# Performance work log

Measured on AMD Instinct MI355X. Metric: run time of the kernel, lower is better.

Reference implementation:

```python
import jax, jax.numpy as jnp
import numpy as np

N_NODES = 100000
N_USERS = 60000
N_MOVIES = 40000
N_EDGES = 1200000
D_IN = 64
D_EMB = 64


def setup_inputs() -> dict:
    key = jax.random.key(0)
    ks = jax.random.split(key, 6)
    x = jax.random.normal(ks[0], (N_NODES, D_IN), dtype=jnp.float32)
    edge_index = jax.random.randint(ks[1], (2, N_EDGES), 0, N_NODES, dtype=jnp.int64)
    # Glorot-ish init for the two GCNConv linear weights
    W1 = jax.random.normal(ks[2], (D_IN, D_EMB), dtype=jnp.float32) * (1.0 / np.sqrt(D_IN))
    b1 = jnp.zeros((D_EMB,), dtype=jnp.float32)
    W2 = jax.random.normal(ks[3], (D_EMB, D_EMB), dtype=jnp.float32) * (1.0 / np.sqrt(D_EMB))
    b2 = jnp.zeros((D_EMB,), dtype=jnp.float32)
    return {"x": x, "edge_index": edge_index, "W1": W1, "b1": b1, "W2": W2, "b2": b2}


def gcn_conv(x, W, b, src, dst):
    """PyG GCNConv: D^{-1/2}(A+I)D^{-1/2} X W + b with symmetric norm and self-loops."""
    h = x @ W  # [N, D_out]
    ones = jnp.ones(src.shape[0], dtype=h.dtype)
    # degree includes self-loop (+1)
    deg = jax.ops.segment_sum(ones, dst, num_segments=N_NODES) + 1.0
    dinv = jax.lax.rsqrt(deg)  # [N]
    coef = dinv[src] * dinv[dst]  # [E]
    agg = jax.ops.segment_sum(h[src] * coef[:, None], dst, num_segments=N_NODES)
    # self-loop contribution: norm = dinv[i]^2
    return agg + h * (dinv * dinv)[:, None] + b


def reference(x, edge_index, W1, b1, W2, b2):
    src, dst = edge_index[0], edge_index[1]
    h = gcn_conv(x, W1, b1, src, dst)
    h = jax.nn.relu(h)  # dropout is identity in eval mode
    h = gcn_conv(h, W2, b2, src, dst)
    user = h[:N_USERS]
    movie = h[N_USERS:N_USERS + N_MOVIES]
    return user, movie, h
```

## Files before the change

### kernel.cpp

```cpp
#include <hip/hip_runtime.h>

#define NN 100000
#define NE 1200000
#define DD 64
#define NPART 8
#define PSZ (NN / NPART)
#define EPB 4096
#define NCHUNK ((NE + EPB - 1) / EPB)
#define SCH 1024
#define SNB ((NN + SCH - 1) / SCH)

#define KCH3 96
#define CEH3 (NE / KCH3)
#define P3 4
#define BINS3 (NN / P3)
#define BINW3 (BINS3 / 4)
#define KSEG 4
#define KPS (KCH3 / KSEG)
#define NW4 (NN / 4)
#define HISTB (KCH3 * P3)
#define GEMMB ((NN + 255) / 256)

static __device__ __forceinline__ unsigned short f2bf(float f) {
    unsigned int u = __float_as_uint(f);
    u += 0x7fffu + ((u >> 16) & 1u);
    return (unsigned short)(u >> 16);
}
static __device__ __forceinline__ float bf_lo(unsigned int u) { return __uint_as_float(u << 16); }
static __device__ __forceinline__ float bf_hi(unsigned int u) { return __uint_as_float(u & 0xffff0000u); }

__global__ __launch_bounds__(1024) void k_histgemm(const int* __restrict__ dst,
                                                   unsigned char* __restrict__ H,
                                                   unsigned char* __restrict__ rank8,
                                                   const float* __restrict__ X,
                                                   const float* __restrict__ W,
                                                   unsigned short* __restrict__ Hb) {
    __shared__ union SM {
        unsigned int bins[BINW3];
        struct { float4 Ws4[64][16]; float Xs[64][68]; } g;
    } sm;
    int t = threadIdx.x;
    if (blockIdx.x < HISTB) {
        int k = blockIdx.x >> 2;
        int p = blockIdx.x & 3;
        for (int i = t; i < BINW3; i += 1024) sm.bins[i] = 0u;
        __syncthreads();
        int lo = p * BINS3;
        int beg = k * CEH3;
        for (int e4 = beg + t * 4; e4 < beg + CEH3; e4 += 4096) {
            int4 d4 = *(const int4*)&dst[e4];
            int dd[4] = {d4.x, d4.y, d4.z, d4.w};
#pragma unroll
            for (int j = 0; j < 4; ++j) {
                unsigned int r = (unsigned int)(dd[j] - lo);
                if (r < (unsigned int)BINS3) {
                    unsigned int sh = (r & 3u) << 3;
                    unsigned int old = atomicAdd(&sm.bins[r >> 2], 1u << sh);
                    rank8[e4 + j] = (unsigned char)((old >> sh) & 0xffu);
                }
            }
        }
        __syncthreads();
        unsigned int* Hw = (unsigned int*)(H + (size_t)k * NN + lo);
        for (int i = t; i < BINW3; i += 1024) Hw[i] = sm.bins[i];
    } else {
        const float4* W4 = (const float4*)W;
        sm.g.Ws4[t >> 4][t & 15] = W4[t];
        int row0 = (int)(blockIdx.x - HISTB) * 256;
        const float4* X4 = (const float4*)X;
        int r = t >> 4, q = t & 15;
#pragma unroll
        for (int s = 0; s < 4; ++s) {
            int row = row0 + s * 64 + r;
            float4 v = make_float4(0.f, 0.f, 0.f, 0.f);
            if (row < NN) v = X4[row * 16 + q];
            __syncthreads();
            *((float4*)&sm.g.Xs[r][q * 4]) = v;
            __syncthreads();
            float4 acc = make_float4(0.f, 0.f, 0.f, 0.f);
#pragma unroll 4
            for (int k = 0; k < 64; ++k) {
                float4 w = sm.g.Ws4[k][q];
                float x = sm.g.Xs[r][k];
                acc.x += x * w.x; acc.y += x * w.y; acc.z += x * w.z; acc.w += x * w.w;
            }
            if (row < NN) {
                ushort4 o;
                o.x = f2bf(acc.x); o.y = f2bf(acc.y); o.z = f2bf(acc.z); o.w = f2bf(acc.w);
                *((ushort4*)&Hb[(size_t)row * 64 + q * 4]) = o;
            }
        }
    }
}

__global__ __launch_bounds__(256) void k_cseg_sum(const unsigned int* __restrict__ H32,
                                                  unsigned int* __restrict__ aux) {
    int wd = blockIdx.x * 256 + threadIdx.x;
    int seg = blockIdx.y;
    if (wd >= NW4) return;
    unsigned int s = 0;
#pragma unroll
    for (int k = 0; k < KPS; ++k)
        s += H32[(size_t)(seg * KPS + k) * NW4 + wd];
    aux[seg * NW4 + wd] = s;
}

__global__ __launch_bounds__(256) void k_cseg_scan2(unsigned int* __restrict__ H32,
                                                    const unsigned int* __restrict__ aux,
                                                    int* __restrict__ rowptr,
                                                    int* __restrict__ part,
                                                    float* __restrict__ dinv) {
    __shared__ int wsum[4];
    int t = threadIdx.x;
    int wd = blockIdx.x * 256 + t;
    int seg = blockIdx.y;
    bool valid = wd < NW4;
    unsigned int s = 0;
    if (valid) {
        unsigned int base = 0;
        for (int i = 0; i < seg; ++i) base += aux[i * NW4 + wd];
        s = base;
#pragma unroll
        for (int k = 0; k < KPS; ++k) {
            size_t idx = (size_t)(seg * KPS + k) * NW4 + wd;
            unsigned int v = H32[idx];
            H32[idx] = s;
            s += v;
        }
    }
    if (seg != KSEG - 1) return;
    int d0 = valid ? (int)(s & 0xffu) : 0;
    int d1 = valid ? (int)((s >> 8) & 0xffu) : 0;
    int d2 = valid ? (int)((s >> 16) & 0xffu) : 0;
    int d3 = valid ? (int)(s >> 24) : 0;
    int idx = blockIdx.x * SCH + t * 4;
    if (valid) {
        float4 dv;
        dv.x = rsqrtf((float)d0 + 1.0f);
        dv.y = rsqrtf((float)d1 + 1.0f);
        dv.z = rsqrtf((float)d2 + 1.0f);
        dv.w = rsqrtf((float)d3 + 1.0f);
        *(float4*)&dinv[idx] = dv;
    }
    int ssum = d0 + d1 + d2 + d3;
    int lane = t & 63;
    int incl = ssum;
#pragma unroll
    for (int off = 1; off < 64; off <<= 1) {
        int v = __shfl_up(incl, off);
        if (lane >= off) incl += v;
    }
    int wv = t >> 6;
    if (lane == 63) wsum[wv] = incl;
    __syncthreads();
    int woff = 0;
#pragma unroll
    for (int i = 0; i < 4; ++i) if (i < wv) woff += wsum[i];
    int excl = woff + incl - ssum;
    if (valid) {
        int4 rp = make_int4(excl, excl + d0, excl + d0 + d1, excl + d0 + d1 + d2);
        *(int4*)&rowptr[idx] = rp;
    }
    if (t == 255) part[blockIdx.x] = woff + incl;
}

__global__ __launch_bounds__(128) void k_scan_part(int* __restrict__ part, int* __restrict__ rowptr) {
    __shared__ int sm[128];
    int t = threadIdx.x;
    int v = (t < SNB) ? part[t] : 0;
    sm[t] = v;
    __syncthreads();
    for (int off = 1; off < 128; off <<= 1) {
        int add = (t >= off) ? sm[t - off] : 0;
        __syncthreads();
        sm[t] += add;
        __syncthreads();
    }
    if (t == SNB - 1) rowptr[NN] = v;
    if (t < SNB) part[t] = sm[t] - v;
}

__global__ __launch_bounds__(256) void k_fill4(const int* __restrict__ src,
                                               const int* __restrict__ dst,
                                               const unsigned char* __restrict__ rank8,
                                               const unsigned char* __restrict__ H,
                                               const int* __restrict__ rowptr,
                                               const int* __restrict__ part,
                                               const float* __restrict__ dinv,
                                               int2* __restrict__ cc) {
    int e4 = (blockIdx.x * 256 + threadIdx.x) * 4;
    if (e4 >= NE) return;
    int4 d4 = *(const int4*)&dst[e4];
    int4 s4 = *(const int4*)&src[e4];
    unsigned int r4 = *(const unsigned int*)&rank8[e4];
    int dd[4] = {d4.x, d4.y, d4.z, d4.w};
    int ss[4] = {s4.x, s4.y, s4.z, s4.w};
    int k = e4 / CEH3;
#pragma unroll
    for (int j = 0; j < 4; ++j) {
        int d = dd[j], s = ss[j];
        int base = rowptr[d] + part[d >> 10] + (int)H[(size_t)k * NN + d];
        int pos = base + (int)((r4 >> (8 * j)) & 0xffu);
        cc[pos] = make_int2(s, __float_as_int(dinv[s] * dinv[d]));
    }
}

__global__ void k_hist_rank(const int* __restrict__ dst, int* __restrict__ degi,
                            int* __restrict__ rank, int ne) {
    int i = blockIdx.x * blockDim.x + threadIdx.x;
    if (i < ne) rank[i] = atomicAdd(&degi[dst[i]], 1);
}

__global__ __launch_bounds__(256) void k_scan_local(const int* __restrict__ degi,
                                                    int* __restrict__ rowptr,
                                                    int* __restrict__ part,
                                                    float* __restrict__ dinv) {
    __shared__ int wsum[4];
    int t = threadIdx.x;
    int idx = blockIdx.x * SCH + t * 4;
    int d0 = 0, d1 = 0, d2 = 0, d3 = 0;
    if (idx + 3 < NN) {
        int4 v = *(const int4*)&degi[idx];
        d0 = v.x; d1 = v.y; d2 = v.z; d3 = v.w;
        float4 dv;
        dv.x = rsqrtf((float)d0 + 1.0f);
        dv.y = rsqrtf((float)d1 + 1.0f);
        dv.z = rsqrtf((float)d2 + 1.0f);
        dv.w = rsqrtf((float)d3 + 1.0f);
        *(float4*)&dinv[idx] = dv;
    } else {
        if (idx     < NN) { d0 = degi[idx];     dinv[idx]     = rsqrtf((float)d0 + 1.0f); }
        if (idx + 1 < NN) { d1 = degi[idx + 1]; dinv[idx + 1] = rsqrtf((float)d1 + 1.0f); }
        if (idx + 2 < NN) { d2 = degi[idx + 2]; dinv[idx + 2] = rsqrtf((float)d2 + 1.0f); }
        if (idx + 3 < NN) { d3 = degi[idx + 3]; dinv[idx + 3] = rsqrtf((float)d3 + 1.0f); }
    }
    int s = d0 + d1 + d2 + d3;
    int lane = t & 63;
    int incl = s;
#pragma unroll
    for (int off = 1; off < 64; off <<= 1) {
        int v = __shfl_up(incl, off);
        if (lane >= off) incl += v;
    }
    int wv = t >> 6;
    if (lane == 63) wsum[wv] = incl;
    __syncthreads();
    int woff = 0;
#pragma unroll
    for (int i = 0; i < 4; ++i) if (i < wv) woff += wsum[i];
    int excl = woff + incl - s;
    if (idx     < NN) rowptr[idx]     = excl;
    if (idx + 1 < NN) rowptr[idx + 1] = excl + d0;
    if (idx + 2 < NN) rowptr[idx + 2] = excl + d0 + d1;
    if (idx + 3 < NN) rowptr[idx + 3] = excl + d0 + d1 + d2;
    if (t == 255) part[blockIdx.x] = woff + incl;
}

__global__ void k_scan_add(int* __restrict__ rowptr, const int* __restrict__ part) {
    int i = blockIdx.x * blockDim.x + threadIdx.x;
    if (i < NN) rowptr[i] += part[i >> 10];
    if (i == 0) rowptr[NN] = NE;
}

__global__ void k_fill_rank(const int* __restrict__ src, const int* __restrict__ dst,
                            const int* __restrict__ rank, const int* __restrict__ rowptr,
                            int* __restrict__ csr_src, int ne) {
    int e = blockIdx.x * blockDim.x + threadIdx.x;
    if (e < ne) csr_src[rowptr[dst[e]] + rank[e]] = src[e];
}

__global__ __launch_bounds__(256) void k_pack(const int* __restrict__ rowptr,
                                              const int* __restrict__ csr,
                                              const float* __restrict__ dinv,
                                              int2* __restrict__ cc) {
    int n = blockIdx.x * 256 + threadIdx.x;
    if (n >= NN) return;
    float dn = dinv[n];
    for (int e = rowptr[n]; e < rowptr[n + 1]; ++e) {
        int s = csr[e];
        cc[e] = make_int2(s, __float_as_int(dinv[s] * dn));
    }
}

__global__ __launch_bounds__(256) void k_gemm_bf(const float* __restrict__ X,
                                                 const float* __restrict__ W,
                                                 unsigned short* __restrict__ Hb,
                                                 int nrows) {
    __shared__ float4 Ws4[64][16];
    __shared__ float  Xs[64][68];
    int tid = threadIdx.x;
    const float4* W4 = (const float4*)W;
    for (int i = tid; i < 64 * 16; i += 256) Ws4[i >> 4][i & 15] = W4[i];
    int row0 = blockIdx.x * 64;
    const float4* X4 = (const float4*)X;
    for (int i = tid; i < 64 * 16; i += 256) {
        int r = i >> 4, q = i & 15;
        int row = row0 + r;
        float4 v = make_float4(0.f, 0.f, 0.f, 0.f);
        if (row < nrows) v = X4[row * 16 + q];
        *((float4*)&Xs[r][q * 4]) = v;
    }
    __syncthreads();
    int c4 = tid & 15;
    int rg = tid >> 4;
    float4 acc0 = make_float4(0.f, 0.f, 0.f, 0.f);
    float4 acc1 = acc0, acc2 = acc0, acc3 = acc0;
#pragma unroll 4
    for (int k = 0; k < 64; ++k) {
        float4 w = Ws4[k][c4];
        float x0 = Xs[rg * 4 + 0][k];
        float x1 = Xs[rg * 4 + 1][k];
        float x2 = Xs[rg * 4 + 2][k];
        float x3 = Xs[rg * 4 + 3][k];
        acc0.x += x0 * w.x; acc0.y += x0 * w.y; acc0.z += x0 * w.z; acc0.w += x0 * w.w;
        acc1.x += x1 * w.x; acc1.y += x1 * w.y; acc1.z += x1 * w.z; acc1.w += x1 * w.w;
        acc2.x += x2 * w.x; acc2.y += x2 * w.y; acc2.z += x2 * w.z; acc2.w += x2 * w.w;
        acc3.x += x3 * w.x; acc3.y += x3 * w.y; acc3.z += x3 * w.z; acc3.w += x3 * w.w;
    }
    float4 accs[4] = {acc0, acc1, acc2, acc3};
#pragma unroll
    for (int i = 0; i < 4; ++i) {
        int row = row0 + rg * 4 + i;
        if (row < nrows) {
            ushort4 o;
            o.x = f2bf(accs[i].x); o.y = f2bf(accs[i].y);
            o.z = f2bf(accs[i].z); o.w = f2bf(accs[i].w);
            *((ushort4*)&Hb[row * 64 + c4 * 4]) = o;
        }
    }
}

static __device__ __forceinline__ void gather8(const unsigned short* __restrict__ Hb,
                                               const int2* __restrict__ cc,
                                               int e0, int deg, int dmax, int cg,
                                               float acc[8]) {
#define LDE(T, S, C) { bool _v = (T) < deg; int2 _w = _v ? cc[e0 + (T)] : make_int2(0, 0); \
                       S = _w.x; C = __int_as_float(_w.y); }
#define GAT(U, S) U = *(const uint4*)(Hb + (size_t)(S) * 64 + cg * 8);
#define CONS(U, C) { acc[0] += bf_lo(U.x) * (C);  acc[1] += bf_hi(U.x) * (C); \
                     acc[2] += bf_lo(U.y) * (C);  acc[3] += bf_hi(U.y) * (C); \
                     acc[4] += bf_lo(U.z) * (C);  acc[5] += bf_hi(U.z) * (C); \
                     acc[6] += bf_lo(U.w) * (C);  acc[7] += bf_hi(U.w) * (C); }
    int s0, s1, s2, s3; float c0, c1, c2, c3;
    LDE(0, s0, c0); LDE(1, s1, c1); LDE(2, s2, c2); LDE(3, s3, c3);
    uint4 u0, u1, u2, u3;
    GAT(u0, s0); GAT(u1, s1); GAT(u2, s2); GAT(u3, s3);
    for (int t = 0; t < dmax; t += 4) {
        int sn0, sn1, sn2, sn3; float cn0, cn1, cn2, cn3;
        LDE(t + 4, sn0, cn0); LDE(t + 5, sn1, cn1);
        LDE(t + 6, sn2, cn2); LDE(t + 7, sn3, cn3);
        CONS(u0, c0); GAT(u0, sn0); c0 = cn0;
        CONS(u1, c1); GAT(u1, sn1); c1 = cn1;
        CONS(u2, c2); GAT(u2, sn2); c2 = cn2;
        CONS(u3, c3); GAT(u3, sn3); c3 = cn3;
    }
#undef LDE
#undef GAT
#undef CONS
}

__global__ __launch_bounds__(256) void k_reduce_g2(const unsigned short* __restrict__ Hb,
                                                   const int* __restrict__ rowptr,
                                                   const int* __restrict__ part,
                                                   const int2* __restrict__ cc,
                                                   const float* __restrict__ dinv,
                                                   const float* __restrict__ bias,
                                                   const float* __restrict__ W2,
                                                   unsigned short* __restrict__ Hb2) {
    __shared__ float4 Ws4[64][16];
    __shared__ float rows[32][68];
    int t = threadIdx.x;
    const float4* W4 = (const float4*)W2;
    for (int i = t; i < 1024; i += 256) Ws4[i >> 4][i & 15] = W4[i];

    int n = blockIdx.x * 32 + (t >> 3);
    int cg = t & 7;
    bool nv = n < NN;
    float din = nv ? dinv[n] : 0.f;
    uint4 us = make_uint4(0u, 0u, 0u, 0u);
    int e0 = 0, deg = 0;
    if (nv) {
        us = *(const uint4*)(Hb + (size_t)n * 64 + cg * 8);
        int rp0 = rowptr[n] + part[n >> 10];
        int rp1 = rowptr[n + 1] + part[(n + 1) >> 10];
        e0 = rp0; deg = rp1 - rp0;
    }
    int dmax = deg;
    dmax = max(dmax, __shfl_xor(dmax, 8));
    dmax = max(dmax, __shfl_xor(dmax, 16));
    dmax = max(dmax, __shfl_xor(dmax, 32));

    float acc[8];
#pragma unroll
    for (int j = 0; j < 8; ++j) acc[j] = 0.f;
    gather8(Hb, cc, e0, deg, dmax, cg, acc);

    float ddn = din * din;
    float4 b0 = *(const float4*)(bias + cg * 8);
    float4 b1 = *(const float4*)(bias + cg * 8 + 4);
    float4 o0, o1;
    o0.x = fmaxf(acc[0] + bf_lo(us.x) * ddn + b0.x, 0.f);
    o0.y = fmaxf(acc[1] + bf_hi(us.x) * ddn + b0.y, 0.f);
    o0.z = fmaxf(acc[2] + bf_lo(us.y) * ddn + b0.z, 0.f);
    o0.w = fmaxf(acc[3] + bf_hi(us.y) * ddn + b0.w, 0.f);
    o1.x = fmaxf(acc[4] + bf_lo(us.z) * ddn + b1.x, 0.f);
    o1.y = fmaxf(acc[5] + bf_hi(us.z) * ddn + b1.y, 0.f);
    o1.z = fmaxf(acc[6] + bf_lo(us.w) * ddn + b1.z, 0.f);
    o1.w = fmaxf(acc[7] + bf_hi(us.w) * ddn + b1.w, 0.f);
    int node = t >> 3;
    *(float4*)&rows[node][cg * 8]     = o0;
    *(float4*)&rows[node][cg * 8 + 4] = o1;
    __syncthreads();

    int c2 = t & 7;
    float a0 = 0.f, a1 = 0.f, a2 = 0.f, a3 = 0.f, a4 = 0.f, a5 = 0.f, a6 = 0.f, a7 = 0.f;
#pragma unroll 4
    for (int k = 0; k < 64; ++k) {
        float r = rows[node][k];
        float4 w0 = Ws4[k][c2 * 2];
        float4 w1 = Ws4[k][c2 * 2 + 1];
        a0 += r * w0.x; a1 += r * w0.y; a2 += r * w0.z; a3 += r * w0.w;
        a4 += r * w1.x; a5 += r * w1.y; a6 += r * w1.z; a7 += r * w1.w;
    }
    if (nv) {
        uint4 pk;
        pk.x = (unsigned int)f2bf(a0) | ((unsigned int)f2bf(a1) << 16);
        pk.y = (unsigned int)f2bf(a2) | ((unsigned int)f2bf(a3) << 16);
        pk.z = (unsigned int)f2bf(a4) | ((unsigned int)f2bf(a5) << 16);
        pk.w = (unsigned int)f2bf(a6) | ((unsigned int)f2bf(a7) << 16);
        *(uint4*)&Hb2[(size_t)n * 64 + c2 * 8] = pk;
    }
}

__global__ __launch_bounds__(256) void k_reduce2(const unsigned short* __restrict__ Hb,
                                                 const int* __restrict__ rowptr,
                                                 const int* __restrict__ part,
                                                 const int2* __restrict__ cc,
                                                 const float* __restrict__ dinv,
                                                 const float* __restrict__ bias,
                                                 float* __restrict__ out0,
                                                 float* __restrict__ out1) {
    int n = blockIdx.x * 32 + (threadIdx.x >> 3);
    if (n >= NN) return;
    int cg = threadIdx.x & 7;
    float din = dinv[n];
    uint4 us = *(const uint4*)(Hb + (size_t)n * 64 + cg * 8);
    int rp0 = rowptr[n] + part[n >> 10];
    int rp1 = rowptr[n + 1] + part[(n + 1) >> 10];
    int e0 = rp0, deg = rp1 - rp0;
    int dmax = deg;
    dmax = max(dmax, __shfl_xor(dmax, 8));
    dmax = max(dmax, __shfl_xor(dmax, 16));
    dmax = max(dmax, __shfl_xor(dmax, 32));

    float acc[8];
#pragma unroll
    for (int j = 0; j < 8; ++j) acc[j] = 0.f;
    gather8(Hb, cc, e0, deg, dmax, cg, acc);

    float ddn = din * din;
    float4 b0 = *(const float4*)(bias + cg * 8);
    float4 b1 = *(const float4*)(bias + cg * 8 + 4);
    float4 o0, o1;
    o0.x = acc[0] + bf_lo(us.x) * ddn + b0.x;
    o0.y = acc[1] + bf_hi(us.x) * ddn + b0.y;
    o0.z = acc[2] + bf_lo(us.y) * ddn + b0.z;
    o0.w = acc[3] + bf_hi(us.y) * ddn + b0.w;
    o1.x = acc[4] + bf_lo(us.z) * ddn + b1.x;
    o1.y = acc[5] + bf_hi(us.z) * ddn + b1.y;
    o1.z = acc[6] + bf_lo(us.w) * ddn + b1.z;
    o1.w = acc[7] + bf_hi(us.w) * ddn + b1.w;
    *(float4*)(out0 + (size_t)n * 64 + cg * 8)     = o0;
    *(float4*)(out0 + (size_t)n * 64 + cg * 8 + 4) = o1;
    *(float4*)(out1 + (size_t)n * 64 + cg * 8)     = o0;
    *(float4*)(out1 + (size_t)n * 64 + cg * 8 + 4) = o1;
}

extern "C" void kernel_launch(void* const* d_in, const int* in_sizes, int n_in,
                              void* d_out, int out_size, void* d_ws, size_t ws_size,
                              hipStream_t stream) {
    const float* x  = (const float*)d_in[0];
    const int*   ei = (const int*)d_in[1];
    const float* W1 = (const float*)d_in[2];
    const float* b1 = (const float*)d_in[3];
    const float* W2 = (const float*)d_in[4];
    const float* b2 = (const float*)d_in[5];
    const int* src = ei;
    const int* dst = ei + NE;

    float* A = (float*)d_out;
    float* B = (float*)d_out + (size_t)NN * DD;

    char* w = (char*)d_ws;
    size_t off = 0;
    auto alloc = [&](size_t bytes) { void* p = w + off; off += (bytes + 255) & ~(size_t)255; return p; };
    float* dinv   = (float*)alloc(NN * sizeof(float));
    int*   degi   = (int*)  alloc(NN * sizeof(int));
    int*   cnt    = (int*)  alloc(NN * sizeof(int));
    int*   rowptr = (int*)  alloc((NN + 1) * sizeof(int));
    int*   part   = (int*)  alloc(512 * sizeof(int));
    int*   csr    = (int*)  alloc(NE * sizeof(int));
    int2*  cc     = (int2*) alloc(NE * sizeof(int2));
    void*  uni    = alloc((size_t)NN * DD * sizeof(unsigned short));
    unsigned char* Hh    = (unsigned char*)uni;
    unsigned char* rank8 = (unsigned char*)uni + (size_t)KCH3 * NN;
    unsigned short* Bb2  = (unsigned short*)uni;
    unsigned short* Bb1 = (unsigned short*)alloc((size_t)NN * DD * sizeof(unsigned short));
    int* rank = (int*)Bb1;
    size_t off_total = off;

    bool new_path = (ws_size >= off_total);

    if (new_path) {
        k_histgemm<<<HISTB + GEMMB, 1024, 0, stream>>>(dst, Hh, rank8, x, W1, Bb1);
        dim3 cgrid((NW4 + 255) / 256, KSEG);
        k_cseg_sum<<<cgrid, 256, 0, stream>>>((unsigned int*)Hh, (unsigned int*)cnt);
        k_cseg_scan2<<<cgrid, 256, 0, stream>>>((unsigned int*)Hh, (const unsigned int*)cnt,
                                                rowptr, part, dinv);
        k_scan_part<<<1, 128, 0, stream>>>(part, rowptr);
        k_fill4<<<(NE / 4 + 255) / 256, 256, 0, stream>>>(src, dst, rank8, Hh, rowptr, part, dinv, cc);
        k_reduce_g2<<<(NN + 31) / 32, 256, 0, stream>>>(Bb1, rowptr, part, cc, dinv, b1, W2, Bb2);
        k_reduce2<<<(NN + 31) / 32, 256, 0, stream>>>(Bb2, rowptr, part, cc, dinv, b2, A, B);
    } else {
        hipMemsetAsync(degi, 0, NN * sizeof(int), stream);
        k_hist_rank<<<(NE + 255) / 256, 256, 0, stream>>>(dst, degi, rank, NE);
        k_scan_local<<<SNB, 256, 0, stream>>>(degi, rowptr, part, dinv);
        k_scan_part<<<1, 128, 0, stream>>>(part, rowptr);
        k_scan_add<<<(NN + 255) / 256, 256, 0, stream>>>(rowptr, part);
        hipMemsetAsync(part, 0, 512 * sizeof(int), stream);
        k_fill_rank<<<(NE + 255) / 256, 256, 0, stream>>>(src, dst, rank, rowptr, csr, NE);
        k_pack<<<(NN + 255) / 256, 256, 0, stream>>>(rowptr, csr, dinv, cc);
        k_gemm_bf<<<(NN + 63) / 64, 256, 0, stream>>>(x, W1, Bb1, NN);
        k_reduce_g2<<<(NN + 31) / 32, 256, 0, stream>>>(Bb1, rowptr, part, cc, dinv, b1, W2, Bb2);
        k_reduce2<<<(NN + 31) / 32, 256, 0, stream>>>(Bb2, rowptr, part, cc, dinv, b2, A, B);
    }
}
```

Baseline: 233.9 us.

## Sort nodes by degree within scan blocks to balance gather wavefronts

The scan kernel now builds a per-block counting sort of nodes by in-degree (capped at 63) and writes a permutation. Both aggregation kernels read node ids through this permutation, so the 8 nodes sharing a wavefront have similar degrees and the dmax-bounded gather loop wastes fewer lane iterations. The cost is extra shared-memory atomics in the scan, an indirection load, and scattered row writes. Bounds checks are removed, which relies on NN being a multiple of 32.

```diff
diff --git a/kernel.cpp b/kernel.cpp
--- a/kernel.cpp
+++ b/kernel.cpp
@@ -3,10 +3,6 @@
 #define NN 100000
 #define NE 1200000
 #define DD 64
-#define NPART 8
-#define PSZ (NN / NPART)
-#define EPB 4096
-#define NCHUNK ((NE + EPB - 1) / EPB)
 #define SCH 1024
 #define SNB ((NN + SCH - 1) / SCH)
 
@@ -109,8 +105,10 @@
                                                     const unsigned int* __restrict__ aux,
                                                     int* __restrict__ rowptr,
                                                     int* __restrict__ part,
-                                                    float* __restrict__ dinv) {
+                                                    float* __restrict__ dinv,
+                                                    int* __restrict__ perm) {
     __shared__ int wsum[4];
+    __shared__ int hist[64];
     int t = threadIdx.x;
     int wd = blockIdx.x * 256 + t;
     int seg = blockIdx.y;
@@ -152,16 +150,41 @@
     }
     int wv = t >> 6;
     if (lane == 63) wsum[wv] = incl;
+    if (t < 64) hist[t] = 0;
     __syncthreads();
     int woff = 0;
 #pragma unroll
     for (int i = 0; i < 4; ++i) if (i < wv) woff += wsum[i];
     int excl = woff + incl - ssum;
+    int r0 = 0, r1 = 0, r2 = 0, r3 = 0;
     if (valid) {
         int4 rp = make_int4(excl, excl + d0, excl + d0 + d1, excl + d0 + d1 + d2);
         *(int4*)&rowptr[idx] = rp;
+        r0 = atomicAdd(&hist[min(d0, 63)], 1);
+        r1 = atomicAdd(&hist[min(d1, 63)], 1);
+        r2 = atomicAdd(&hist[min(d2, 63)], 1);
+        r3 = atomicAdd(&hist[min(d3, 63)], 1);
     }
     if (t == 255) part[blockIdx.x] = woff + incl;
+    __syncthreads();
+    if (t < 64) {
+        int v = hist[t];
+        int inc = v;
+#pragma unroll
+        for (int off = 1; off < 64; off <<= 1) {
+            int u = __shfl_up(inc, off);
+            if (t >= off) inc += u;
+        }
+        hist[t] = inc - v;
+    }
+    __syncthreads();
+    if (valid) {
+        int base = blockIdx.x * SCH;
+        perm[base + hist[min(d0, 63)] + r0] = idx;
+        perm[base + hist[min(d1, 63)] + r1] = idx + 1;
+        perm[base + hist[min(d2, 63)] + r2] = idx + 2;
+        perm[base + hist[min(d3, 63)] + r3] = idx + 3;
+    }
 }
 
 __global__ __launch_bounds__(128) void k_scan_part(int* __restrict__ part, int* __restrict__ rowptr) {
@@ -280,6 +303,11 @@
         int s = csr[e];
         cc[e] = make_int2(s, __float_as_int(dinv[s] * dn));
     }
+}
+
+__global__ void k_iota(int* __restrict__ perm) {
+    int i = blockIdx.x * blockDim.x + threadIdx.x;
+    if (i < NN) perm[i] = i;
 }
 
 __global__ __launch_bounds__(256) void k_gemm_bf(const float* __restrict__ X,
@@ -364,6 +392,7 @@
                                                    const int* __restrict__ part,
                                                    const int2* __restrict__ cc,
                                                    const float* __restrict__ dinv,
+                                                   const int* __restrict__ perm,
                                                    const float* __restrict__ bias,
                                                    const float* __restrict__ W2,
                                                    unsigned short* __restrict__ Hb2) {
@@ -373,18 +402,13 @@
     const float4* W4 = (const float4*)W2;
     for (int i = t; i < 1024; i += 256) Ws4[i >> 4][i & 15] = W4[i];
 
-    int n = blockIdx.x * 32 + (t >> 3);
+    int n = perm[blockIdx.x * 32 + (t >> 3)];
     int cg = t & 7;
-    bool nv = n < NN;
-    float din = nv ? dinv[n] : 0.f;
-    uint4 us = make_uint4(0u, 0u, 0u, 0u);
-    int e0 = 0, deg = 0;
-    if (nv) {
-        us = *(const uint4*)(Hb + (size_t)n * 64 + cg * 8);
-        int rp0 = rowptr[n] + part[n >> 10];
-        int rp1 = rowptr[n + 1] + part[(n + 1) >> 10];
-        e0 = rp0; deg = rp1 - rp0;
-    }
+    float din = dinv[n];
+    uint4 us = *(const uint4*)(Hb + (size_t)n * 64 + cg * 8);
+    int rp0 = rowptr[n] + part[n >> 10];
+    int rp1 = rowptr[n + 1] + part[(n + 1) >> 10];
+    int e0 = rp0, deg = rp1 - rp0;
     int dmax = deg;
     dmax = max(dmax, __shfl_xor(dmax, 8));
     dmax = max(dmax, __shfl_xor(dmax, 16));
@@ -422,14 +446,12 @@
         a0 += r * w0.x; a1 += r * w0.y; a2 += r * w0.z; a3 += r * w0.w;
         a4 += r * w1.x; a5 += r * w1.y; a6 += r * w1.z; a7 += r * w1.w;
     }
-    if (nv) {
-        uint4 pk;
-        pk.x = (unsigned int)f2bf(a0) | ((unsigned int)f2bf(a1) << 16);
-        pk.y = (unsigned int)f2bf(a2) | ((unsigned int)f2bf(a3) << 16);
-        pk.z = (unsigned int)f2bf(a4) | ((unsigned int)f2bf(a5) << 16);
-        pk.w = (unsigned int)f2bf(a6) | ((unsigned int)f2bf(a7) << 16);
-        *(uint4*)&Hb2[(size_t)n * 64 + c2 * 8] = pk;
-    }
+    uint4 pk;
+    pk.x = (unsigned int)f2bf(a0) | ((unsigned int)f2bf(a1) << 16);
+    pk.y = (unsigned int)f2bf(a2) | ((unsigned int)f2bf(a3) << 16);
+    pk.z = (unsigned int)f2bf(a4) | ((unsigned int)f2bf(a5) << 16);
+    pk.w = (unsigned int)f2bf(a6) | ((unsigned int)f2bf(a7) << 16);
+    *(uint4*)&Hb2[(size_t)n * 64 + c2 * 8] = pk;
 }
 
 __global__ __launch_bounds__(256) void k_reduce2(const unsigned short* __restrict__ Hb,
@@ -437,11 +459,11 @@
                                                  const int* __restrict__ part,
                                                  const int2* __restrict__ cc,
                                                  const float* __restrict__ dinv,
+                                                 const int* __restrict__ perm,
                                                  const float* __restrict__ bias,
                                                  float* __restrict__ out0,
                                                  float* __restrict__ out1) {
-    int n = blockIdx.x * 32 + (threadIdx.x >> 3);
-    if (n >= NN) return;
+    int n = perm[blockIdx.x * 32 + (threadIdx.x >> 3)];
     int cg = threadIdx.x & 7;
     float din = dinv[n];
     uint4 us = *(const uint4*)(Hb + (size_t)n * 64 + cg * 8);
@@ -499,6 +521,7 @@
     int*   cnt    = (int*)  alloc(NN * sizeof(int));
     int*   rowptr = (int*)  alloc((NN + 1) * sizeof(int));
     int*   part   = (int*)  alloc(512 * sizeof(int));
+    int*   perm   = (int*)  alloc(NN * sizeof(int));
     int*   csr    = (int*)  alloc(NE * sizeof(int));
     int2*  cc     = (int2*) alloc(NE * sizeof(int2));
     void*  uni    = alloc((size_t)NN * DD * sizeof(unsigned short));
@@ -516,11 +539,11 @@
         dim3 cgrid((NW4 + 255) / 256, KSEG);
         k_cseg_sum<<<cgrid, 256, 0, stream>>>((unsigned int*)Hh, (unsigned int*)cnt);
         k_cseg_scan2<<<cgrid, 256, 0, stream>>>((unsigned int*)Hh, (const unsigned int*)cnt,
-                                                rowptr, part, dinv);
+                                                rowptr, part, dinv, perm);
         k_scan_part<<<1, 128, 0, stream>>>(part, rowptr);
         k_fill4<<<(NE / 4 + 255) / 256, 256, 0, stream>>>(src, dst, rank8, Hh, rowptr, part, dinv, cc);
-        k_reduce_g2<<<(NN + 31) / 32, 256, 0, stream>>>(Bb1, rowptr, part, cc, dinv, b1, W2, Bb2);
-        k_reduce2<<<(NN + 31) / 32, 256, 0, stream>>>(Bb2, rowptr, part, cc, dinv, b2, A, B);
+        k_reduce_g2<<<NN / 32, 256, 0, stream>>>(Bb1, rowptr, part, cc, dinv, perm, b1, W2, Bb2);
+        k_reduce2<<<NN / 32, 256, 0, stream>>>(Bb2, rowptr, part, cc, dinv, perm, b2, A, B);
     } else {
         hipMemsetAsync(degi, 0, NN * sizeof(int), stream);
         k_hist_rank<<<(NE + 255) / 256, 256, 0, stream>>>(dst, degi, rank, NE);
@@ -530,8 +553,9 @@
         hipMemsetAsync(part, 0, 512 * sizeof(int), stream);
         k_fill_rank<<<(NE + 255) / 256, 256, 0, stream>>>(src, dst, rank, rowptr, csr, NE);
         k_pack<<<(NN + 255) / 256, 256, 0, stream>>>(rowptr, csr, dinv, cc);
+        k_iota<<<(NN + 255) / 256, 256, 0, stream>>>(perm);
         k_gemm_bf<<<(NN + 63) / 64, 256, 0, stream>>>(x, W1, Bb1, NN);
-        k_reduce_g2<<<(NN + 31) / 32, 256, 0, stream>>>(Bb1, rowptr, part, cc, dinv, b1, W2, Bb2);
-        k_reduce2<<<(NN + 31) / 32, 256, 0, stream>>>(Bb2, rowptr, part, cc, dinv, b2, A, B);
-    }
-}
+        k_reduce_g2<<<NN / 32, 256, 0, stream>>>(Bb1, rowptr, part, cc, dinv, perm, b1, W2, Bb2);
+        k_reduce2<<<NN / 32, 256, 0, stream>>>(Bb2, rowptr, part, cc, dinv, perm, b2, A, B);
+    }
+}
```

Measured after the change: 245.7 us. +5.0%, slower.
